# Optimization experiments

Measured on AMD Instinct MI355X. Metric: run time of the kernel, lower is better.

The kernel has to match this reference:

```python
import jax, jax.numpy as jnp
import numpy as np

# Config constants (mirrors VQConfig)
N_CODEBOOKS = 4
NUM_EMBS = 512
EMB_DIM = 32
NUM_LATENTS = 64
DECAY = 0.999
COMMITMENT_COST = 0.25
EPSILON = 1e-05
BATCH = 1024


def setup_inputs() -> dict:
    key = jax.random.key(0)
    k1, k2 = jax.random.split(key)
    x = jax.random.normal(k1, (BATCH, N_CODEBOOKS * EMB_DIM * NUM_LATENTS), dtype=jnp.float32)
    # embedding.uniform_(-1/M*5, 1/M*5)
    lim = 5.0 / NUM_EMBS
    embedding = jax.random.uniform(k2, (N_CODEBOOKS, NUM_EMBS, EMB_DIM), dtype=jnp.float32,
                                   minval=-lim, maxval=lim)
    ema_count = jnp.zeros((N_CODEBOOKS, NUM_EMBS), dtype=jnp.float32)
    ema_weight = embedding  # clone of embedding at init
    return {"x": x, "embedding": embedding, "ema_count": ema_count, "ema_weight": ema_weight}


def reference(x, embedding, ema_count, ema_weight):
    N, M, D = embedding.shape
    B = x.shape[0]
    L = x.shape[1] // (N * D)  # num_discrete_latents (H dim; W = 1)
    T = B * L  # flattened positions per codebook

    # x.view(B, N*D, L, 1).view(B, N, D, H, W).permute(1,0,3,4,2) -> [N,B,L,1,D]
    xr = x.reshape(B, N, D, L, 1).transpose(1, 0, 3, 4, 2)
    x_flat = jax.lax.stop_gradient(xr).reshape(N, T, D)

    e_sq = jnp.sum(embedding ** 2, axis=2)                       # [N, M]
    x_sq = jnp.sum(x_flat ** 2, axis=2, keepdims=True)           # [N, T, 1]
    xe = jnp.einsum('ntd,nmd->ntm', x_flat, embedding)           # [N, T, M]
    distances = e_sq[:, None, :] + x_sq - 2.0 * xe
    indices = jnp.argmin(distances, axis=-1)                     # [N, T] int

    # gather: quantized[n, t] = embedding[n, indices[n, t]]
    quantized = jnp.take_along_axis(embedding, indices[..., None], axis=1)  # [N,T,D]
    quantized_r = quantized.reshape(N, B, L, 1, D)

    # one-hot sums without materializing one-hot: scatter-add via segment_sum
    flat_idx = (indices + jnp.arange(N, dtype=indices.dtype)[:, None] * M).reshape(-1)
    counts = jax.ops.segment_sum(jnp.ones((N * T,), jnp.float32), flat_idx,
                                 num_segments=N * M).reshape(N, M)
    dw = jax.ops.segment_sum(x_flat.reshape(N * T, D), flat_idx,
                             num_segments=N * M).reshape(N, M, D)

    # EMA updates (training branch)
    new_ema_count = DECAY * ema_count + (1.0 - DECAY) * counts
    n_tot = jnp.sum(new_ema_count, axis=-1, keepdims=True)
    new_ema_count = (new_ema_count + EPSILON) / (n_tot + M * EPSILON) * n_tot
    new_ema_weight = DECAY * ema_weight + (1.0 - DECAY) * dw
    new_embedding = new_ema_weight / new_ema_count[..., None]

    # commitment loss + straight-through estimator
    e_latent_loss = jnp.mean((xr - jax.lax.stop_gradient(quantized_r)) ** 2)
    loss = COMMITMENT_COST * e_latent_loss
    quantized_st = jax.lax.stop_gradient(quantized_r) + xr - jax.lax.stop_gradient(xr)

    # perplexity
    avg_probs = counts / T                                       # [N, M]
    perplexity = jnp.exp(-jnp.sum(avg_probs * jnp.log(avg_probs + 1e-10), axis=-1))
    perplexity_sum = jnp.sum(perplexity)

    # [N,B,L,1,D] -> permute(1,0,4,2,3) -> [B,N,D,L,1] -> flatten
    z_q = quantized_st.transpose(1, 0, 4, 2, 3).reshape(B, N * D * L)
    indices_out = indices.reshape(N, B, L, 1).transpose(1, 0, 2, 3)  # [B,N,L,1]

    return (z_q, loss, perplexity_sum, indices_out,
            new_embedding, new_ema_count, new_ema_weight)
```

## Files before the change

kernel.cpp:

```cpp
#include <hip/hip_runtime.h>

#define NCB 4
#define M 512
#define D 32
#define L 64
#define B 1024
#define XS (NCB * D * L)
#define QM 128

#define ZQ_OFF   0
#define LOSS_OFF 8388608
#define PERP_OFF 8388609
#define IDX_OFF  8388610
#define NEMB_OFF 8650754
#define NEC_OFF  8716290
#define NWE_OFF  8718338

#define WS_COUNTS 0
#define WS_DW     2048
#define WS_SSE    67584
#define WS_FLOATS (WS_SSE + 1)

#define REFINE_EPS 1e-4f

#define NP_SUM32(sq, res) do {                                              \
    float r0=(sq)[0], r1=(sq)[1], r2=(sq)[2], r3=(sq)[3];                   \
    float r4=(sq)[4], r5=(sq)[5], r6=(sq)[6], r7=(sq)[7];                   \
    r0 += (sq)[8];  r1 += (sq)[9];  r2 += (sq)[10]; r3 += (sq)[11];         \
    r4 += (sq)[12]; r5 += (sq)[13]; r6 += (sq)[14]; r7 += (sq)[15];         \
    r0 += (sq)[16]; r1 += (sq)[17]; r2 += (sq)[18]; r3 += (sq)[19];         \
    r4 += (sq)[20]; r5 += (sq)[21]; r6 += (sq)[22]; r7 += (sq)[23];         \
    r0 += (sq)[24]; r1 += (sq)[25]; r2 += (sq)[26]; r3 += (sq)[27];         \
    r4 += (sq)[28]; r5 += (sq)[29]; r6 += (sq)[30]; r7 += (sq)[31];         \
    (res) = ((r0 + r1) + (r2 + r3)) + ((r4 + r5) + (r6 + r7));              \
} while (0)

__global__ __launch_bounds__(256, 4) void vq_main(
    const float* __restrict__ x, const float* __restrict__ emb,
    float* __restrict__ out, float* __restrict__ ws)
{
#pragma clang fp contract(off)
    __shared__ float s_emb[QM * D];
    __shared__ float s_esq[M];

    const int tid = threadIdx.x;
    const int lane = tid & 63;
    const int bid = blockIdx.x;
    const int n  = bid >> 8;
    const int t  = ((bid & 255) << 8) + tid;
    const float* __restrict__ embn = emb + n * (M * D);

#pragma unroll
    for (int k = 0; k < 2; ++k) {
        const int r = tid + k * 256;
        const float* ep = embn + r * D;
        float sq[D];
#pragma unroll
        for (int d = 0; d < D; ++d) { const float e = ep[d]; sq[d] = e * e; }
        NP_SUM32(sq, s_esq[r]);
    }

    const int b = t >> 6, l = t & 63;
    float xr[D];
    {
        const float* xp = x + (size_t)b * XS + n * (D * L) + l;
#pragma unroll
        for (int d = 0; d < D; ++d) xr[d] = xp[d * L];
    }

    float xsq;
    {
        float sq[D];
#pragma unroll
        for (int d = 0; d < D; ++d) sq[d] = xr[d] * xr[d];
        NP_SUM32(sq, xsq);
    }

    float best = 3.4e38f, secnd = 3.4e38f;
    int   bi = 0;

    for (int qtr = 0; qtr < 4; ++qtr) {
        __syncthreads();
        {
            const float4* src = (const float4*)(embn + qtr * (QM * D));
            float4* dst = (float4*)s_emb;
#pragma unroll
            for (int k = 0; k < 4; ++k) dst[tid + k * 256] = src[tid + k * 256];
        }
        __syncthreads();

        for (int mm = 0; mm < QM; ++mm) {
            const float4* e4 = (const float4*)(s_emb + mm * D);
            const int m = qtr * QM + mm;
            const float es = s_esq[m];
            float a0 = 0.f, a1 = 0.f, a2 = 0.f, a3 = 0.f;
#pragma unroll
            for (int q = 0; q < 8; q += 4) {
                const float4 v0 = e4[q], v1 = e4[q+1], v2 = e4[q+2], v3 = e4[q+3];
                a0 = fmaf(v0.x, xr[q*4+ 0], a0); a0 = fmaf(v0.y, xr[q*4+ 1], a0);
                a0 = fmaf(v0.z, xr[q*4+ 2], a0); a0 = fmaf(v0.w, xr[q*4+ 3], a0);
                a1 = fmaf(v1.x, xr[q*4+ 4], a1); a1 = fmaf(v1.y, xr[q*4+ 5], a1);
                a1 = fmaf(v1.z, xr[q*4+ 6], a1); a1 = fmaf(v1.w, xr[q*4+ 7], a1);
                a2 = fmaf(v2.x, xr[q*4+ 8], a2); a2 = fmaf(v2.y, xr[q*4+ 9], a2);
                a2 = fmaf(v2.z, xr[q*4+10], a2); a2 = fmaf(v2.w, xr[q*4+11], a2);
                a3 = fmaf(v3.x, xr[q*4+12], a3); a3 = fmaf(v3.y, xr[q*4+13], a3);
                a3 = fmaf(v3.z, xr[q*4+14], a3); a3 = fmaf(v3.w, xr[q*4+15], a3);
            }
            const float s = fmaf(-2.f, ((a0 + a1) + (a2 + a3)), es);
            const bool lt = s < best;
            secnd = lt ? best : fminf(secnd, s);
            best  = lt ? s : best;
            bi    = lt ? m : bi;
        }
    }

    {
        unsigned long long mask = __ballot(secnd - best < REFINE_EPS);
        while (mask) {
            const int src = __ffsll(mask) - 1;
            mask &= mask - 1;
            float xb[D];
#pragma unroll
            for (int d = 0; d < D; ++d) xb[d] = __shfl(xr[d], src, 64);
            const float xsb = __shfl(xsq, src, 64);
            float bs = 3.4e38f; int bm = M;
            for (int mb = 0; mb < 8; ++mb) {
                const int m = mb * 64 + lane;
                const float4* e4 = (const float4*)(embn + m * D);
                float ee[D];
#pragma unroll
                for (int q = 0; q < 8; ++q) {
                    const float4 v = e4[q];
                    ee[q*4+0] = v.x; ee[q*4+1] = v.y; ee[q*4+2] = v.z; ee[q*4+3] = v.w;
                }
                float lnk[4];
#pragma unroll
                for (int il = 0; il < 4; ++il) {
                    float c;
                    c = xb[12+il] * ee[12+il];
                    c = xb[ 8+il] * ee[ 8+il] + c;
                    c = xb[ 4+il] * ee[ 4+il] + c;
                    c = xb[ 0+il] * ee[ 0+il] + c;
                    c = xb[28+il] * ee[28+il] + c;
                    c = xb[24+il] * ee[24+il] + c;
                    c = xb[20+il] * ee[20+il] + c;
                    c = xb[16+il] * ee[16+il] + c;
                    lnk[il] = c;
                }
                const float xe   = (lnk[0] + lnk[1]) + (lnk[2] + lnk[3]);
                const float a1   = s_esq[m] + xsb;
                const float dist = a1 - 2.f * xe;
                if (dist < bs || (dist == bs && m < bm)) { bs = dist; bm = m; }
            }
#pragma unroll
            for (int off = 32; off > 0; off >>= 1) {
                const float os = __shfl_xor(bs, off, 64);
                const int   om = __shfl_xor(bm, off, 64);
                if (os < bs || (os == bs && om < bm)) { bs = os; bm = om; }
            }
            if (lane == src) bi = bm;
        }
    }

    float sse = 0.f;
    {
        const float* q = embn + bi * D;
        float* zq = out + ZQ_OFF + (size_t)b * XS + n * (D * L) + l;
#pragma unroll
        for (int d = 0; d < D; ++d) {
            const float qv = q[d];
            zq[d * L] = qv;
            const float diff = xr[d] - qv;
            sse = fmaf(diff, diff, sse);
        }
        out[IDX_OFF + ((size_t)b * NCB + n) * L + l] = (float)bi;
        unsafeAtomicAdd(&ws[WS_COUNTS + n * M + bi], 1.0f);
        float* dwp = ws + WS_DW + (size_t)(n * M + bi) * D;
#pragma unroll
        for (int d = 0; d < D; ++d) unsafeAtomicAdd(&dwp[d], xr[d]);
    }

#pragma unroll
    for (int off = 32; off > 0; off >>= 1) sse += __shfl_down(sse, off, 64);
    if (lane == 0) unsafeAtomicAdd(&ws[WS_SSE], sse);
}

__global__ __launch_bounds__(256) void vq_finalize(
    const float* __restrict__ ema_count, const float* __restrict__ ema_weight,
    const float* __restrict__ ws, float* __restrict__ out)
{
    const int n = blockIdx.x, tid = threadIdx.x;
    __shared__ float s_nec[M];
    __shared__ float s_red[16];

    float pre[2], tot = 0.f, ent = 0.f;
#pragma unroll
    for (int k = 0; k < 2; ++k) {
        const int m = tid + k * 256;
        const float c = ws[WS_COUNTS + n * M + m];
        pre[k] = 0.999f * ema_count[n * M + m] + 0.001f * c;
        tot += pre[k];
        const float p = c * (1.f / 65536.f);
        ent += p * logf(p + 1e-10f);
    }
#pragma unroll
    for (int off = 32; off > 0; off >>= 1) {
        tot += __shfl_down(tot, off, 64);
        ent += __shfl_down(ent, off, 64);
    }
    const int w = tid >> 6;
    if ((tid & 63) == 0) { s_red[w] = tot; s_red[8 + w] = ent; }
    __syncthreads();
    tot = s_red[0] + s_red[1] + s_red[2] + s_red[3];
    ent = s_red[8] + s_red[9] + s_red[10] + s_red[11];

    if (tid == 0) unsafeAtomicAdd(&out[PERP_OFF], expf(-ent));
    if (n == 0 && tid == 0) out[LOSS_OFF] = 0.25f * ws[WS_SSE] * (1.f / 8388608.f);

#pragma unroll
    for (int k = 0; k < 2; ++k) {
        const int m = tid + k * 256;
        const float nec = (pre[k] + 1e-5f) / (tot + M * 1e-5f) * tot;
        out[NEC_OFF + n * M + m] = nec;
        s_nec[m] = nec;
    }
    __syncthreads();

    for (int e = tid; e < M * D; e += 256) {
        const int m = e >> 5;
        const float wv = 0.999f * ema_weight[n * (M * D) + e] + 0.001f * ws[WS_DW + n * (M * D) + e];
        out[NWE_OFF + n * (M * D) + e] = wv;
        out[NEMB_OFF + n * (M * D) + e] = wv / s_nec[m];
    }
}

extern "C" void kernel_launch(void* const* d_in, const int* in_sizes, int n_in,
                              void* d_out, int out_size, void* d_ws, size_t ws_size,
                              hipStream_t stream) {
    const float* x          = (const float*)d_in[0];
    const float* embedding  = (const float*)d_in[1];
    const float* ema_count  = (const float*)d_in[2];
    const float* ema_weight = (const float*)d_in[3];
    float* out = (float*)d_out;
    float* ws  = (float*)d_ws;

    hipMemsetAsync(ws, 0, WS_FLOATS * sizeof(float), stream);
    hipMemsetAsync((char*)d_out + (size_t)LOSS_OFF * sizeof(float), 0, 2 * sizeof(float), stream);

    vq_main<<<dim3(1024), dim3(256), 0, stream>>>(x, embedding, out, ws);
    vq_finalize<<<dim3(NCB), dim3(256), 0, stream>>>(ema_count, ema_weight, ws, out);
}
```

Before: 882.5 us.

## Read codebook directly via uniform scalar loads instead of LDS staging

Removes the shared-memory staging of codebook quarters and the per-block recomputation of embedding squared norms. The norms now come from a small precomputation kernel written to workspace. The main loop reads embedding rows straight from global memory, and since every lane reads the same row the compiler can use scalar (SMEM) loads through the scalar cache. This drops the block barriers and LDS traffic, but each block now depends on scalar-cache hit rates and pays one extra kernel launch.

```diff
diff --git a/kernel.cpp b/kernel.cpp
--- a/kernel.cpp
+++ b/kernel.cpp
@@ -6,7 +6,6 @@
 #define L 64
 #define B 1024
 #define XS (NCB * D * L)
-#define QM 128
 
 #define ZQ_OFF   0
 #define LOSS_OFF 8388608
@@ -19,7 +18,8 @@
 #define WS_COUNTS 0
 #define WS_DW     2048
 #define WS_SSE    67584
-#define WS_FLOATS (WS_SSE + 1)
+#define WS_ESQ    67585
+#define WS_FLOATS (WS_ESQ + NCB * M)
 
 #define REFINE_EPS 1e-4f
 
@@ -35,30 +35,33 @@
     (res) = ((r0 + r1) + (r2 + r3)) + ((r4 + r5) + (r6 + r7));              \
 } while (0)
 
+__global__ __launch_bounds__(256) void vq_esq(
+    const float* __restrict__ emb, float* __restrict__ ws)
+{
+#pragma clang fp contract(off)
+    const int r = blockIdx.x * 256 + threadIdx.x;
+    const float* ep = emb + (size_t)r * D;
+    float sq[D];
+#pragma unroll
+    for (int d = 0; d < D; ++d) { const float e = ep[d]; sq[d] = e * e; }
+    float res;
+    NP_SUM32(sq, res);
+    ws[WS_ESQ + r] = res;
+}
+
 __global__ __launch_bounds__(256, 4) void vq_main(
     const float* __restrict__ x, const float* __restrict__ emb,
+    const float* __restrict__ esq,
     float* __restrict__ out, float* __restrict__ ws)
 {
 #pragma clang fp contract(off)
-    __shared__ float s_emb[QM * D];
-    __shared__ float s_esq[M];
-
     const int tid = threadIdx.x;
     const int lane = tid & 63;
     const int bid = blockIdx.x;
     const int n  = bid >> 8;
     const int t  = ((bid & 255) << 8) + tid;
     const float* __restrict__ embn = emb + n * (M * D);
-
-#pragma unroll
-    for (int k = 0; k < 2; ++k) {
-        const int r = tid + k * 256;
-        const float* ep = embn + r * D;
-        float sq[D];
-#pragma unroll
-        for (int d = 0; d < D; ++d) { const float e = ep[d]; sq[d] = e * e; }
-        NP_SUM32(sq, s_esq[r]);
-    }
+    const float* __restrict__ esqn = esq + n * M;
 
     const int b = t >> 6, l = t & 63;
     float xr[D];
@@ -79,39 +82,25 @@
     float best = 3.4e38f, secnd = 3.4e38f;
     int   bi = 0;
 
-    for (int qtr = 0; qtr < 4; ++qtr) {
-        __syncthreads();
-        {
-            const float4* src = (const float4*)(embn + qtr * (QM * D));
-            float4* dst = (float4*)s_emb;
-#pragma unroll
-            for (int k = 0; k < 4; ++k) dst[tid + k * 256] = src[tid + k * 256];
+    for (int m = 0; m < M; ++m) {
+        const float* __restrict__ ep = embn + m * D;
+        float a0 = 0.f, a1 = 0.f, a2 = 0.f, a3 = 0.f;
+#pragma unroll
+        for (int h = 0; h < D; h += 16) {
+            a0 = fmaf(ep[h+ 0], xr[h+ 0], a0); a0 = fmaf(ep[h+ 1], xr[h+ 1], a0);
+            a0 = fmaf(ep[h+ 2], xr[h+ 2], a0); a0 = fmaf(ep[h+ 3], xr[h+ 3], a0);
+            a1 = fmaf(ep[h+ 4], xr[h+ 4], a1); a1 = fmaf(ep[h+ 5], xr[h+ 5], a1);
+            a1 = fmaf(ep[h+ 6], xr[h+ 6], a1); a1 = fmaf(ep[h+ 7], xr[h+ 7], a1);
+            a2 = fmaf(ep[h+ 8], xr[h+ 8], a2); a2 = fmaf(ep[h+ 9], xr[h+ 9], a2);
+            a2 = fmaf(ep[h+10], xr[h+10], a2); a2 = fmaf(ep[h+11], xr[h+11], a2);
+            a3 = fmaf(ep[h+12], xr[h+12], a3); a3 = fmaf(ep[h+13], xr[h+13], a3);
+            a3 = fmaf(ep[h+14], xr[h+14], a3); a3 = fmaf(ep[h+15], xr[h+15], a3);
         }
-        __syncthreads();
-
-        for (int mm = 0; mm < QM; ++mm) {
-            const float4* e4 = (const float4*)(s_emb + mm * D);
-            const int m = qtr * QM + mm;
-            const float es = s_esq[m];
-            float a0 = 0.f, a1 = 0.f, a2 = 0.f, a3 = 0.f;
-#pragma unroll
-            for (int q = 0; q < 8; q += 4) {
-                const float4 v0 = e4[q], v1 = e4[q+1], v2 = e4[q+2], v3 = e4[q+3];
-                a0 = fmaf(v0.x, xr[q*4+ 0], a0); a0 = fmaf(v0.y, xr[q*4+ 1], a0);
-                a0 = fmaf(v0.z, xr[q*4+ 2], a0); a0 = fmaf(v0.w, xr[q*4+ 3], a0);
-                a1 = fmaf(v1.x, xr[q*4+ 4], a1); a1 = fmaf(v1.y, xr[q*4+ 5], a1);
-                a1 = fmaf(v1.z, xr[q*4+ 6], a1); a1 = fmaf(v1.w, xr[q*4+ 7], a1);
-                a2 = fmaf(v2.x, xr[q*4+ 8], a2); a2 = fmaf(v2.y, xr[q*4+ 9], a2);
-                a2 = fmaf(v2.z, xr[q*4+10], a2); a2 = fmaf(v2.w, xr[q*4+11], a2);
-                a3 = fmaf(v3.x, xr[q*4+12], a3); a3 = fmaf(v3.y, xr[q*4+13], a3);
-                a3 = fmaf(v3.z, xr[q*4+14], a3); a3 = fmaf(v3.w, xr[q*4+15], a3);
-            }
-            const float s = fmaf(-2.f, ((a0 + a1) + (a2 + a3)), es);
-            const bool lt = s < best;
-            secnd = lt ? best : fminf(secnd, s);
-            best  = lt ? s : best;
-            bi    = lt ? m : bi;
-        }
+        const float s = fmaf(-2.f, ((a0 + a1) + (a2 + a3)), esqn[m]);
+        const bool lt = s < best;
+        secnd = lt ? best : fminf(secnd, s);
+        best  = lt ? s : best;
+        bi    = lt ? m : bi;
     }
 
     {
@@ -148,8 +137,8 @@
                     lnk[il] = c;
                 }
                 const float xe   = (lnk[0] + lnk[1]) + (lnk[2] + lnk[3]);
-                const float a1   = s_esq[m] + xsb;
-                const float dist = a1 - 2.f * xe;
+                const float a1v  = esqn[m] + xsb;
+                const float dist = a1v - 2.f * xe;
                 if (dist < bs || (dist == bs && m < bm)) { bs = dist; bm = m; }
             }
 #pragma unroll
@@ -244,9 +233,10 @@
     float* out = (float*)d_out;
     float* ws  = (float*)d_ws;
 
-    hipMemsetAsync(ws, 0, WS_FLOATS * sizeof(float), stream);
+    hipMemsetAsync(ws, 0, (WS_SSE + 1) * sizeof(float), stream);
     hipMemsetAsync((char*)d_out + (size_t)LOSS_OFF * sizeof(float), 0, 2 * sizeof(float), stream);
 
-    vq_main<<<dim3(1024), dim3(256), 0, stream>>>(x, embedding, out, ws);
+    vq_esq<<<dim3(NCB * M / 256), dim3(256), 0, stream>>>(embedding, ws);
+    vq_main<<<dim3(1024), dim3(256), 0, stream>>>(x, embedding, ws + WS_ESQ, out, ws);
     vq_finalize<<<dim3(NCB), dim3(256), 0, stream>>>(ema_count, ema_weight, ws, out);
 }
```

New measurement: 900.9 us. 1.02x slower.
